# Performance work log

Measured on AMD Instinct MI355X. Metric: run time of the kernel, lower is better.

Reference implementation:

```python
import jax, jax.numpy as jnp
import numpy as np

NEG = -1e9

def gat_layer(x, edge_mask, W, al, ar, rW, b, act):
    # x: (B, N, Fin); edge_mask: (B, N, N) bool, edge u->v at [b,u,v]
    B, N, _ = x.shape
    H, D = al.shape
    f = (x @ W).reshape(B, N, H, D)                      # (B,N,H,D)
    el = jnp.einsum('bnhd,hd->bnh', f, al)               # src term
    er = jnp.einsum('bnhd,hd->bnh', f, ar)               # dst term
    # e[b,u,v,h] = LeakyReLU(el[src=u] + er[dst=v]), slope 0.2 (dgl default)
    e = jax.nn.leaky_relu(el[:, :, None, :] + er[:, None, :, :], 0.2)
    logits = jnp.where(edge_mask[..., None], e, NEG)
    # masked, empty-column-safe softmax over incoming edges (axis=1 = src u)
    m = jnp.max(logits, axis=1, keepdims=True)
    p = jnp.exp(logits - m) * edge_mask[..., None]
    alpha = p / jnp.clip(jnp.sum(p, axis=1, keepdims=True), 1e-9)
    out = jnp.einsum('buvh,buhd->bvhd', alpha, f)        # scatter-sum to dst
    res = (x @ rW).reshape(B, N, H, D)                   # residual projection
    out = out + res + b.reshape(H, D)
    return act(out) if act is not None else out


def setup_inputs() -> dict:
    key = jax.random.key(0)
    ks = jax.random.split(key, 12)
    n, c, h, w = 16, 64, 32, 32
    num_s, hid, H = 64, 64, 4
    seg = jax.random.normal(ks[0], (n, c, h, w), dtype=jnp.float32)
    adj = jax.random.normal(ks[1], (n, h * w, h * w), dtype=jnp.float32)
    s = 0.1
    return {
        'seg': seg, 'adj': adj,
        'W0': jax.random.normal(ks[2], (num_s, H * hid), dtype=jnp.float32) * s,
        'al0': jax.random.normal(ks[3], (H, hid), dtype=jnp.float32) * s,
        'ar0': jax.random.normal(ks[4], (H, hid), dtype=jnp.float32) * s,
        'rW0': jax.random.normal(ks[5], (num_s, H * hid), dtype=jnp.float32) * s,
        'b0': jnp.zeros((H * hid,), dtype=jnp.float32),
        'W1': jax.random.normal(ks[6], (H * hid, H * num_s), dtype=jnp.float32) * s,
        'al1': jax.random.normal(ks[7], (H, num_s), dtype=jnp.float32) * s,
        'ar1': jax.random.normal(ks[8], (H, num_s), dtype=jnp.float32) * s,
        'rW1': jax.random.normal(ks[9], (H * hid, H * num_s), dtype=jnp.float32) * s,
        'b1': jnp.zeros((H * num_s,), dtype=jnp.float32),
    }


def reference(seg, adj, W0, al0, ar0, rW0, b0, W1, al1, ar1, rW1, b1):
    n, c, h, w = seg.shape
    num_s = W0.shape[0]
    x = seg.reshape(n, -1, num_s)                        # (n, N, num_s)
    k = (h * w) // 6
    topv, _ = jax.lax.top_k(adj, k)
    thr = topv[..., -1]                                  # k-th largest per row
    adj_t = jnp.where(adj >= thr[..., None], adj, 0.0)
    edge_mask = adj_t > 0                                # (n, N, N)
    fea = gat_layer(x, edge_mask, W0, al0, ar0, rW0, b0, jax.nn.elu)
    fea = fea.reshape(n, fea.shape[1], -1)               # flatten heads
    fea = gat_layer(fea, edge_mask, W1, al1, ar1, rW1, b1, None)
    out = fea.mean(axis=2)                               # mean over heads -> (n, N, num_s)
    return out.reshape(n, -1, num_s)
```

## Files before the change

### kernel.cpp

```cpp
#include <hip/hip_runtime.h>
#include <hip/hip_bf16.h>
#include <stdint.h>

#define BB   16
#define NN   1024
#define KSEL 170
#define LOG2E 1.4426950408889634f

typedef __attribute__((ext_vector_type(8))) short short8;
typedef __attribute__((ext_vector_type(4))) short short4v;
typedef __attribute__((ext_vector_type(4))) float f32x4;

static __device__ __forceinline__ short f2bf(float x) {
    __hip_bfloat16 h = __float2bfloat16(x);
    return *reinterpret_cast<short*>(&h);
}
static __device__ __forceinline__ float bf2f(short x) {
    uint32_t u = ((uint32_t)(uint16_t)x) << 16;
    return __uint_as_float(u);
}
static __device__ __forceinline__ float fast_exp2(float x) {
    float r; asm("v_exp_f32 %0, %1" : "=v"(r) : "v"(x)); return r;
}

__global__ __launch_bounds__(256) void k_topk_mask(
    const float* __restrict__ adj, uint64_t* __restrict__ mask)
{
    const int wid = threadIdx.x >> 6, lane = threadIdx.x & 63;
    const int row = blockIdx.x * 4 + wid;
    const float* a = adj + (size_t)row * NN;
    __shared__ uint32_t hist[4][256];
    uint32_t* h = hist[wid];

    uint32_t key[16];
    #pragma unroll
    for (int j = 0; j < 16; ++j) {
        uint32_t u = __float_as_uint(a[lane + j * 64]);
        key[j] = u ^ ((u >> 31) ? 0xFFFFFFFFu : 0x80000000u);
    }

    uint32_t prefix = 0u, kk = KSEL;
    #pragma unroll
    for (int pass = 0; pass < 4; ++pass) {
        const int shift = 24 - 8 * pass;
        const uint32_t hi_mask = pass ? (0xFFFFFFFFu << (shift + 8)) : 0u;
        *(uint4*)&h[lane * 4] = make_uint4(0u, 0u, 0u, 0u);
        __builtin_amdgcn_wave_barrier();
        #pragma unroll
        for (int j = 0; j < 16; ++j)
            if ((key[j] & hi_mask) == prefix)
                atomicAdd(&h[(key[j] >> shift) & 255], 1u);
        __builtin_amdgcn_wave_barrier();
        const uint4 c4 = *(const uint4*)&h[lane * 4];
        const uint32_t T = c4.x + c4.y + c4.z + c4.w;
        uint32_t s = T;
        #pragma unroll
        for (int off = 1; off < 64; off <<= 1) {
            uint32_t v = __shfl_down(s, off);
            s += (lane + off < 64) ? v : 0u;
        }
        const uint32_t E = s - T;
        const uint32_t s3 = c4.w;
        const uint32_t s2 = c4.z + s3;
        const uint32_t s1 = c4.y + s2;
        const uint32_t s0 = c4.x + s1;
        const uint32_t ci[4] = {c4.x, c4.y, c4.z, c4.w};
        const uint32_t si[4] = {s0, s1, s2, s3};
        uint32_t found = 0u, nb = 0u, nk = 0u;
        #pragma unroll
        for (int i = 0; i < 4; ++i) {
            uint32_t incl = E + si[i];
            uint32_t excl = incl - ci[i];
            if (excl < kk && kk <= incl) { found = 1u; nb = (uint32_t)(lane * 4 + i); nk = kk - excl; }
        }
        uint64_t bal = __ballot(found != 0u);
        int wl = __ffsll((unsigned long long)bal) - 1;
        prefix = prefix | ((uint32_t)__shfl((int)nb, wl) << shift);
        kk = (uint32_t)__shfl((int)nk, wl);
    }

    const uint32_t thr_key = prefix;
    #pragma unroll
    for (int j = 0; j < 16; ++j) {
        bool pred = (key[j] >= thr_key) && (key[j] > 0x80000000u);
        uint64_t bal = __ballot(pred);
        if (lane == 0) mask[(size_t)row * 16 + j] = bal;
    }
}

__global__ __launch_bounds__(256) void k_maskT(
    const uint64_t* __restrict__ mask, uint64_t* __restrict__ maskT)
{
    const int tile = blockIdx.x * 4 + (threadIdx.x >> 6);
    const int lane = threadIdx.x & 63;
    const int b  = tile >> 8;
    const int uw = (tile >> 4) & 15;
    const int vw = tile & 15;
    const size_t bN = (size_t)b * NN;
    uint64_t w = mask[(bN + uw * 64 + lane) * 16 + vw];
    uint64_t r_out = 0;
    #pragma unroll
    for (int j = 0; j < 64; ++j) {
        uint64_t r = __ballot((w >> j) & 1ull);
        if (lane == j) r_out = r;
    }
    maskT[(bN + vw * 64 + lane) * 16 + uw] = r_out;
}

__global__ __launch_bounds__(256) void k_prepare(
    const float* __restrict__ W0, const float* __restrict__ rW0,
    const float* __restrict__ W1, const float* __restrict__ rW1,
    const float* __restrict__ seg,
    short* __restrict__ Wt0, short* __restrict__ rWt0,
    short* __restrict__ Wt1, short* __restrict__ rWt1,
    short* __restrict__ xb0)
{
    const int bid = blockIdx.x, t = threadIdx.x;
    if (bid < 64) {
        int idx = bid * 256 + t;
        int o = idx >> 6, k = idx & 63;
        Wt0[idx] = f2bf(W0[(size_t)k * 256 + o]);
    } else if (bid < 128) {
        int idx = (bid - 64) * 256 + t;
        int o = idx >> 6, k = idx & 63;
        rWt0[idx] = f2bf(rW0[(size_t)k * 256 + o]);
    } else if (bid < 384) {
        int idx = (bid - 128) * 256 + t;
        int o = idx >> 8, k = idx & 255;
        Wt1[idx] = f2bf(W1[(size_t)k * 256 + o]);
    } else if (bid < 640) {
        int idx = (bid - 384) * 256 + t;
        int o = idx >> 8, k = idx & 255;
        rWt1[idx] = f2bf(rW1[(size_t)k * 256 + o]);
    } else {
        int i = ((bid - 640) * 256 + t) * 4;
        float4 v = *(const float4*)(seg + i);
        short4v o4;
        o4[0] = f2bf(v.x); o4[1] = f2bf(v.y); o4[2] = f2bf(v.z); o4[3] = f2bf(v.w);
        *(short4v*)(xb0 + i) = o4;
    }
}

template<int K>
__global__ __launch_bounds__(256, 2) void k_features_mfma(
    const short* __restrict__ xb,
    const short* __restrict__ Wt,
    const short* __restrict__ rWt,
    const float* __restrict__ al,
    const float* __restrict__ ar,
    short* __restrict__ ft,
    short* __restrict__ fea,
    float* __restrict__ el_t,
    float* __restrict__ er_t)
{
    const int tid = threadIdx.x, lane = tid & 63, hh = tid >> 6;
    const int l15 = lane & 15, l4 = lane >> 4;
    const int n0 = blockIdx.x * 32;
    const int b_idx = n0 >> 10;
    const int nloc = n0 & (NN - 1);
    const int bh = b_idx * 4 + hh;
    const int XP = K + 8;

    __shared__ short x_lds[32 * (K + 8)];

    const int CH = K / 8;
    #pragma unroll
    for (int c = tid; c < 32 * CH; c += 256) {
        const int row = c / CH, col = c - row * CH;
        *(short8*)&x_lds[row * XP + col * 8] =
            *(const short8*)(xb + ((size_t)n0 + row) * K + col * 8);
    }
    __syncthreads();

    const short* wbase = Wt  + (size_t)(hh * 64 + l15) * K + l4 * 8;
    const short* rbase = rWt + (size_t)(hh * 64 + l15) * K + l4 * 8;
    const size_t qs = (size_t)16 * K;

    f32x4 accf[2][4], accr[2][4];
    #pragma unroll
    for (int s = 0; s < 2; ++s)
        #pragma unroll
        for (int q = 0; q < 4; ++q) {
            accf[s][q] = (f32x4){0.f, 0.f, 0.f, 0.f};
            accr[s][q] = (f32x4){0.f, 0.f, 0.f, 0.f};
        }

    short8 bufW[2][4], bufR[2][4];
    #pragma unroll
    for (int q = 0; q < 4; ++q) {
        bufW[0][q] = *(const short8*)(wbase + q * qs);
        bufR[0][q] = *(const short8*)(rbase + q * qs);
    }

    #pragma unroll
    for (int ks = 0; ks < K / 32; ++ks) {
        const int cur = ks & 1, nxt = cur ^ 1;
        if (ks + 1 < K / 32) {
            #pragma unroll
            for (int q = 0; q < 4; ++q) {
                bufW[nxt][q] = *(const short8*)(wbase + q * qs + (ks + 1) * 32);
                bufR[nxt][q] = *(const short8*)(rbase + q * qs + (ks + 1) * 32);
            }
            __builtin_amdgcn_sched_barrier(0);
        }
        short8 x0 = *(const short8*)&x_lds[l15 * XP + ks * 32 + l4 * 8];
        short8 x1 = *(const short8*)&x_lds[(16 + l15) * XP + ks * 32 + l4 * 8];
        #pragma unroll
        for (int q = 0; q < 4; ++q) {
            accf[0][q] = __builtin_amdgcn_mfma_f32_16x16x32_bf16(x0, bufW[cur][q], accf[0][q], 0, 0, 0);
            accf[1][q] = __builtin_amdgcn_mfma_f32_16x16x32_bf16(x1, bufW[cur][q], accf[1][q], 0, 0, 0);
            accr[0][q] = __builtin_amdgcn_mfma_f32_16x16x32_bf16(bufR[cur][q], x0, accr[0][q], 0, 0, 0);
            accr[1][q] = __builtin_amdgcn_mfma_f32_16x16x32_bf16(bufR[cur][q], x1, accr[1][q], 0, 0, 0);
        }
    }

    #pragma unroll
    for (int s = 0; s < 2; ++s) {
        const int nl = nloc + s * 16;
        #pragma unroll
        for (int q = 0; q < 4; ++q) {
            short4v pk;
            #pragma unroll
            for (int r = 0; r < 4; ++r) pk[r] = f2bf(accf[s][q][r]);
            const int dl = q * 16 + l15;
            const size_t idx = ((size_t)bh << 16)
                             + (size_t)(nl >> 6) * 4096
                             + (size_t)(((nl & 63) >> 3) + (l4 >> 1)) * 512
                             + (size_t)dl * 8 + (l4 & 1) * 4;
            *(short4v*)(ft + idx) = pk;
        }
        float elv[4] = {0.f, 0.f, 0.f, 0.f}, erv[4] = {0.f, 0.f, 0.f, 0.f};
        #pragma unroll
        for (int q = 0; q < 4; ++q) {
            const float alv = al[hh * 64 + q * 16 + l15];
            const float arv = ar[hh * 64 + q * 16 + l15];
            #pragma unroll
            for (int r = 0; r < 4; ++r) {
                elv[r] = fmaf(accf[s][q][r], alv, elv[r]);
                erv[r] = fmaf(accf[s][q][r], arv, erv[r]);
            }
        }
        #pragma unroll
        for (int r = 0; r < 4; ++r) {
            #pragma unroll
            for (int off = 1; off < 16; off <<= 1) {
                elv[r] += __shfl_xor(elv[r], off);
                erv[r] += __shfl_xor(erv[r], off);
            }
        }
        if (l15 == 0) {
            float4 e4, r4;
            e4.x = elv[0] * LOG2E; e4.y = elv[1] * LOG2E;
            e4.z = elv[2] * LOG2E; e4.w = elv[3] * LOG2E;
            r4.x = erv[0] * LOG2E; r4.y = erv[1] * LOG2E;
            r4.z = erv[2] * LOG2E; r4.w = erv[3] * LOG2E;
            *(float4*)(el_t + (size_t)bh * NN + nl + l4 * 4) = e4;
            *(float4*)(er_t + (size_t)bh * NN + nl + l4 * 4) = r4;
        }
        #pragma unroll
        for (int q = 0; q < 4; ++q) {
            short4v pk;
            #pragma unroll
            for (int r = 0; r < 4; ++r) pk[r] = f2bf(accr[s][q][r]);
            *(short4v*)(fea + ((size_t)n0 + s * 16 + l15) * 256 + hh * 64 + q * 16 + l4 * 4) = pk;
        }
    }
}

template<int ELU_ON>
__global__ __launch_bounds__(256, 4) void k_attn(
    const short* __restrict__ ft,
    const float* __restrict__ el_t,
    const float* __restrict__ er_t,
    const uint64_t* __restrict__ maskT,
    const float* __restrict__ bias,
    short* fea)
{
    const int id = blockIdx.x;
    const int swz = (id & 7) * 64 + (id >> 3);
    const int b  = swz >> 5;
    const int h  = (swz >> 3) & 3;
    const int vt = swz & 7;
    const int tid = threadIdx.x;
    const int lane = tid & 63, wid = tid >> 6;
    const int l15 = lane & 15, l4 = lane >> 4;
    const int bh = b * 4 + h;
    const size_t bN = (size_t)b * NN;
    const int v0 = vt * 128;

    __shared__ __align__(16) short f_lds[2][4096];
    __shared__ __align__(16) float el_lds[NN];
    __shared__ __align__(16) uint64_t m_lds[128 * 17];
    __shared__ float smax[4];

    const short* gsrc = ft + ((size_t)bh << 16);

    {
        short8 sa = *(const short8*)(gsrc + tid * 8);
        short8 sb = *(const short8*)(gsrc + 2048 + tid * 8);
        float4 ev4 = ((const float4*)(el_t + (size_t)bh * NN))[tid];
        ((float4*)el_lds)[tid] = ev4;
        float m = fmaxf(fmaxf(ev4.x, ev4.y), fmaxf(ev4.z, ev4.w));
        #pragma unroll
        for (int off = 32; off; off >>= 1) m = fmaxf(m, __shfl_xor(m, off));
        if (lane == 0) smax[wid] = m;
        #pragma unroll
        for (int i = 0; i < 8; ++i) {
            int idx = tid + i * 256;
            m_lds[(idx >> 4) * 17 + (idx & 15)] =
                maskT[(bN + v0 + (idx >> 4)) * 16 + (idx & 15)];
        }
        *(short8*)&f_lds[0][tid * 8] = sa;
        *(short8*)&f_lds[0][2048 + tid * 8] = sb;
    }

    const int vlo = wid * 32 + l15, vhi = vlo + 16;
    const float er_lo = er_t[(size_t)bh * NN + v0 + vlo];
    const float er_hi = er_t[(size_t)bh * NN + v0 + vhi];

    __syncthreads();

    const float emx = fmaxf(fmaxf(smax[0], smax[1]), fmaxf(smax[2], smax[3]));
    const float e0 = emx + er_lo;
    const float cv_lo = fmaxf(e0, 0.2f * e0);
    const float e1 = emx + er_hi;
    const float cv_hi = fmaxf(e1, 0.2f * e1);
    const float c1_lo = er_lo - cv_lo, c2_lo = 0.2f * er_lo - cv_lo;
    const float c1_hi = er_hi - cv_hi, c2_hi = 0.2f * er_hi - cv_hi;

    const uint8_t* mbytes = (const uint8_t*)m_lds;
    const int moff_lo = vlo * 136, moff_hi = vhi * 136;

    short8 ones8;
    #pragma unroll
    for (int i = 0; i < 8; ++i) ones8[i] = (short)0x3F80;

    f32x4 accLo[4], accHi[4];
    #pragma unroll
    for (int i = 0; i < 4; ++i) {
        accLo[i] = (f32x4){0.f, 0.f, 0.f, 0.f};
        accHi[i] = (f32x4){0.f, 0.f, 0.f, 0.f};
    }
    f32x4 dLo = (f32x4){0.f, 0.f, 0.f, 0.f};
    f32x4 dHi = (f32x4){0.f, 0.f, 0.f, 0.f};

    short8 Ra, Rb;
    #pragma unroll 1
    for (int tt = 0; tt < 16; ++tt) {
        if (tt < 15) {
            Ra = *(const short8*)(gsrc + (tt + 1) * 4096 + tid * 8);
            Rb = *(const short8*)(gsrc + (tt + 1) * 4096 + 2048 + tid * 8);
            __builtin_amdgcn_sched_barrier(0);
        }
        const short* fb = f_lds[tt & 1];
        #pragma unroll
        for (int kc = 0; kc < 2; ++kc) {
            const float* ep = &el_lds[tt * 64 + kc * 32 + l4 * 8];
            float4 ev0 = *(const float4*)ep;
            float4 ev1 = *(const float4*)(ep + 4);
            const float ev[8] = {ev0.x, ev0.y, ev0.z, ev0.w, ev1.x, ev1.y, ev1.z, ev1.w};
            uint32_t mLo = mbytes[moff_lo + tt * 8 + kc * 4 + l4];
            uint32_t mHi = mbytes[moff_hi + tt * 8 + kc * 4 + l4];
            short8 aLo, aHi;
            #pragma unroll
            for (int j = 0; j < 8; ++j) {
                float e = ev[j];
                float argL = fmaxf(e + c1_lo, fmaf(0.2f, e, c2_lo));
                float argH = fmaxf(e + c1_hi, fmaf(0.2f, e, c2_hi));
                float pL = ((mLo >> j) & 1u) ? fast_exp2(argL) : 0.f;
                float pH = ((mHi >> j) & 1u) ? fast_exp2(argH) : 0.f;
                aLo[j] = f2bf(pL);
                aHi[j] = f2bf(pH);
            }
            const int fo = (kc * 4 + l4) * 512 + l15 * 8;
            short8 bw0 = *(const short8*)(fb + fo);
            short8 bw1 = *(const short8*)(fb + fo + 128);
            short8 bw2 = *(const short8*)(fb + fo + 256);
            short8 bw3 = *(const short8*)(fb + fo + 384);
            __builtin_amdgcn_s_setprio(1);
            accLo[0] = __builtin_amdgcn_mfma_f32_16x16x32_bf16(aLo, bw0, accLo[0], 0, 0, 0);
            accLo[1] = __builtin_amdgcn_mfma_f32_16x16x32_bf16(aLo, bw1, accLo[1], 0, 0, 0);
            accLo[2] = __builtin_amdgcn_mfma_f32_16x16x32_bf16(aLo, bw2, accLo[2], 0, 0, 0);
            accLo[3] = __builtin_amdgcn_mfma_f32_16x16x32_bf16(aLo, bw3, accLo[3], 0, 0, 0);
            dLo      = __builtin_amdgcn_mfma_f32_16x16x32_bf16(aLo, ones8, dLo, 0, 0, 0);
            accHi[0] = __builtin_amdgcn_mfma_f32_16x16x32_bf16(aHi, bw0, accHi[0], 0, 0, 0);
            accHi[1] = __builtin_amdgcn_mfma_f32_16x16x32_bf16(aHi, bw1, accHi[1], 0, 0, 0);
            accHi[2] = __builtin_amdgcn_mfma_f32_16x16x32_bf16(aHi, bw2, accHi[2], 0, 0, 0);
            accHi[3] = __builtin_amdgcn_mfma_f32_16x16x32_bf16(aHi, bw3, accHi[3], 0, 0, 0);
            dHi      = __builtin_amdgcn_mfma_f32_16x16x32_bf16(aHi, ones8, dHi, 0, 0, 0);
            __builtin_amdgcn_s_setprio(0);
        }
        if (tt < 15) {
            *(short8*)&f_lds[(tt + 1) & 1][tid * 8] = Ra;
            *(short8*)&f_lds[(tt + 1) & 1][2048 + tid * 8] = Rb;
        }
        __syncthreads();
    }

    float rcpLo[4], rcpHi[4];
    #pragma unroll
    for (int r = 0; r < 4; ++r) {
        rcpLo[r] = 1.f / fmaxf(dLo[r], 1e-9f);
        rcpHi[r] = 1.f / fmaxf(dHi[r], 1e-9f);
    }
    #pragma unroll
    for (int dt = 0; dt < 4; ++dt) {
        const int d = dt * 16 + l15;
        const float bv = bias[h * 64 + d];
        #pragma unroll
        for (int r = 0; r < 4; ++r) {
            const int vl = v0 + wid * 32 + l4 * 4 + r;
            const size_t rowL = (bN + vl) * 256 + h * 64 + d;
            float ov = accLo[dt][r] * rcpLo[r] + bf2f(fea[rowL]) + bv;
            if (ELU_ON) ov = ov > 0.f ? ov : __expf(ov) - 1.f;
            fea[rowL] = f2bf(ov);
            const size_t rowH = (bN + vl + 16) * 256 + h * 64 + d;
            float ov2 = accHi[dt][r] * rcpHi[r] + bf2f(fea[rowH]) + bv;
            if (ELU_ON) ov2 = ov2 > 0.f ? ov2 : __expf(ov2) - 1.f;
            fea[rowH] = f2bf(ov2);
        }
    }
}

__global__ __launch_bounds__(256) void k_headmean(
    const short* __restrict__ fea, float* __restrict__ outp)
{
    int i = blockIdx.x * 256 + threadIdx.x;
    int d = i & 63;
    size_t node = (size_t)(i >> 6);
    const short* p = fea + node * 256;
    outp[i] = 0.25f * (bf2f(p[d]) + bf2f(p[64 + d]) + bf2f(p[128 + d]) + bf2f(p[192 + d]));
}

extern "C" void kernel_launch(void* const* d_in, const int* in_sizes, int n_in,
                              void* d_out, int out_size, void* d_ws, size_t ws_size,
                              hipStream_t stream) {
    const float* seg = (const float*)d_in[0];
    const float* adj = (const float*)d_in[1];
    const float* W0  = (const float*)d_in[2];
    const float* al0 = (const float*)d_in[3];
    const float* ar0 = (const float*)d_in[4];
    const float* rW0 = (const float*)d_in[5];
    const float* b0  = (const float*)d_in[6];
    const float* W1  = (const float*)d_in[7];
    const float* al1 = (const float*)d_in[8];
    const float* ar1 = (const float*)d_in[9];
    const float* rW1 = (const float*)d_in[10];
    const float* b1  = (const float*)d_in[11];
    float* out = (float*)d_out;

    char* ws = (char*)d_ws;
    size_t off = 0;
    uint64_t* mask  = (uint64_t*)ws;
    off += (size_t)BB * NN * 16 * 8;
    uint64_t* maskT = (uint64_t*)(ws + off); off += (size_t)BB * NN * 16 * 8;
    short* ftb = (short*)(ws + off); off += (size_t)BB * 256 * NN * 2;
    short* fea = (short*)(ws + off); off += (size_t)BB * NN * 256 * 2;
    short* xb0 = (short*)(ws + off); off += (size_t)BB * NN * 64 * 2;
    char* r0 = (char*)mask;
    short* Wt0  = (short*)r0;                 r0 += 256 * 64 * 2;
    short* rWt0 = (short*)r0;                 r0 += 256 * 64 * 2;
    short* Wt1  = (short*)r0;                 r0 += 256 * 256 * 2;
    short* rWt1 = (short*)r0;                 r0 += 256 * 256 * 2;
    float* el   = (float*)r0;                 r0 += (size_t)BB * 4 * NN * 4;
    float* er   = (float*)r0;                 r0 += (size_t)BB * 4 * NN * 4;

    k_topk_mask<<<BB * NN / 4, 256, 0, stream>>>(adj, mask);
    k_maskT<<<BB * 256 / 4, 256, 0, stream>>>(mask, maskT);
    k_prepare<<<640 + BB * NN * 64 / 1024, 256, 0, stream>>>(
        W0, rW0, W1, rW1, seg, Wt0, rWt0, Wt1, rWt1, xb0);

    k_features_mfma<64><<<BB * NN / 32, 256, 0, stream>>>(xb0, Wt0, rWt0, al0, ar0,
                                                          ftb, fea, el, er);
    k_attn<1><<<512, 256, 0, stream>>>(ftb, el, er, maskT, b0, fea);
    k_features_mfma<256><<<BB * NN / 32, 256, 0, stream>>>(fea, Wt1, rWt1, al1, ar1,
                                                           ftb, fea, el, er);
    k_attn<0><<<512, 256, 0, stream>>>(ftb, el, er, maskT, b1, fea);

    k_headmean<<<BB * NN * 64 / 256, 256, 0, stream>>>(fea, out);
}
```

Before: 159.4 us.

## Shorten topk radix select and halve attention tile per block

The top-k threshold search now runs only two 8-bit radix histogram passes. It then resolves the remaining low 16 bits by repeated wave-wide max-and-count over the candidates that share the prefix, which avoids two histogram passes. The attention kernel now processes 64 destination nodes per block instead of 128 and launches 1024 blocks, giving more parallelism and fewer registers per thread. In exchange, each feature tile is streamed from global memory twice as often. The iterative max loop could also run many times if many keys share the 16-bit prefix.

```diff
diff --git a/kernel.cpp b/kernel.cpp
--- a/kernel.cpp
+++ b/kernel.cpp
@@ -41,9 +41,9 @@
 
     uint32_t prefix = 0u, kk = KSEL;
     #pragma unroll
-    for (int pass = 0; pass < 4; ++pass) {
+    for (int pass = 0; pass < 2; ++pass) {
         const int shift = 24 - 8 * pass;
-        const uint32_t hi_mask = pass ? (0xFFFFFFFFu << (shift + 8)) : 0u;
+        const uint32_t hi_mask = pass ? 0xFF000000u : 0u;
         *(uint4*)&h[lane * 4] = make_uint4(0u, 0u, 0u, 0u);
         __builtin_amdgcn_wave_barrier();
         #pragma unroll
@@ -79,7 +79,34 @@
         kk = (uint32_t)__shfl((int)nk, wl);
     }
 
-    const uint32_t thr_key = prefix;
+    uint32_t sv[16];
+    #pragma unroll
+    for (int j = 0; j < 16; ++j)
+        sv[j] = ((key[j] ^ prefix) >> 16) == 0u ? key[j] : 0u;
+
+    uint32_t thr_key;
+    for (;;) {
+        uint32_t m = 0u;
+        #pragma unroll
+        for (int j = 0; j < 16; ++j) m = m > sv[j] ? m : sv[j];
+        #pragma unroll
+        for (int off = 1; off < 64; off <<= 1) {
+            uint32_t v = __shfl_xor(m, off);
+            m = m > v ? m : v;
+        }
+        if (m == 0u) { thr_key = 0u; break; }
+        uint32_t c = 0u;
+        #pragma unroll
+        for (int j = 0; j < 16; ++j) c += (sv[j] == m) ? 1u : 0u;
+        #pragma unroll
+        for (int off = 1; off < 64; off <<= 1)
+            c += __shfl_xor(c, off);
+        if (kk <= c) { thr_key = m; break; }
+        kk -= c;
+        #pragma unroll
+        for (int j = 0; j < 16; ++j) if (sv[j] == m) sv[j] = 0u;
+    }
+
     #pragma unroll
     for (int j = 0; j < 16; ++j) {
         bool pred = (key[j] >= thr_key) && (key[j] > 0x80000000u);
@@ -277,20 +304,20 @@
     short* fea)
 {
     const int id = blockIdx.x;
-    const int swz = (id & 7) * 64 + (id >> 3);
-    const int b  = swz >> 5;
-    const int h  = (swz >> 3) & 3;
-    const int vt = swz & 7;
+    const int swz = (id & 7) * 128 + (id >> 3);
+    const int b  = swz >> 6;
+    const int h  = (swz >> 4) & 3;
+    const int vt = swz & 15;
     const int tid = threadIdx.x;
     const int lane = tid & 63, wid = tid >> 6;
     const int l15 = lane & 15, l4 = lane >> 4;
     const int bh = b * 4 + h;
     const size_t bN = (size_t)b * NN;
-    const int v0 = vt * 128;
+    const int v0 = vt * 64;
 
     __shared__ __align__(16) short f_lds[2][4096];
     __shared__ __align__(16) float el_lds[NN];
-    __shared__ __align__(16) uint64_t m_lds[128 * 17];
+    __shared__ __align__(16) uint64_t m_lds[64 * 17];
     __shared__ float smax[4];
 
     const short* gsrc = ft + ((size_t)bh << 16);
@@ -305,7 +332,7 @@
         for (int off = 32; off; off >>= 1) m = fmaxf(m, __shfl_xor(m, off));
         if (lane == 0) smax[wid] = m;
         #pragma unroll
-        for (int i = 0; i < 8; ++i) {
+        for (int i = 0; i < 4; ++i) {
             int idx = tid + i * 256;
             m_lds[(idx >> 4) * 17 + (idx & 15)] =
                 maskT[(bN + v0 + (idx >> 4)) * 16 + (idx & 15)];
@@ -314,35 +341,27 @@
         *(short8*)&f_lds[0][2048 + tid * 8] = sb;
     }
 
-    const int vlo = wid * 32 + l15, vhi = vlo + 16;
+    const int vlo = wid * 16 + l15;
     const float er_lo = er_t[(size_t)bh * NN + v0 + vlo];
-    const float er_hi = er_t[(size_t)bh * NN + v0 + vhi];
 
     __syncthreads();
 
     const float emx = fmaxf(fmaxf(smax[0], smax[1]), fmaxf(smax[2], smax[3]));
     const float e0 = emx + er_lo;
     const float cv_lo = fmaxf(e0, 0.2f * e0);
-    const float e1 = emx + er_hi;
-    const float cv_hi = fmaxf(e1, 0.2f * e1);
     const float c1_lo = er_lo - cv_lo, c2_lo = 0.2f * er_lo - cv_lo;
-    const float c1_hi = er_hi - cv_hi, c2_hi = 0.2f * er_hi - cv_hi;
 
     const uint8_t* mbytes = (const uint8_t*)m_lds;
-    const int moff_lo = vlo * 136, moff_hi = vhi * 136;
+    const int moff_lo = vlo * 136;
 
     short8 ones8;
     #pragma unroll
     for (int i = 0; i < 8; ++i) ones8[i] = (short)0x3F80;
 
-    f32x4 accLo[4], accHi[4];
-    #pragma unroll
-    for (int i = 0; i < 4; ++i) {
-        accLo[i] = (f32x4){0.f, 0.f, 0.f, 0.f};
-        accHi[i] = (f32x4){0.f, 0.f, 0.f, 0.f};
-    }
+    f32x4 accLo[4];
+    #pragma unroll
+    for (int i = 0; i < 4; ++i) accLo[i] = (f32x4){0.f, 0.f, 0.f, 0.f};
     f32x4 dLo = (f32x4){0.f, 0.f, 0.f, 0.f};
-    f32x4 dHi = (f32x4){0.f, 0.f, 0.f, 0.f};
 
     short8 Ra, Rb;
     #pragma unroll 1
@@ -360,17 +379,13 @@
             float4 ev1 = *(const float4*)(ep + 4);
             const float ev[8] = {ev0.x, ev0.y, ev0.z, ev0.w, ev1.x, ev1.y, ev1.z, ev1.w};
             uint32_t mLo = mbytes[moff_lo + tt * 8 + kc * 4 + l4];
-            uint32_t mHi = mbytes[moff_hi + tt * 8 + kc * 4 + l4];
-            short8 aLo, aHi;
+            short8 aLo;
             #pragma unroll
             for (int j = 0; j < 8; ++j) {
                 float e = ev[j];
                 float argL = fmaxf(e + c1_lo, fmaf(0.2f, e, c2_lo));
-                float argH = fmaxf(e + c1_hi, fmaf(0.2f, e, c2_hi));
                 float pL = ((mLo >> j) & 1u) ? fast_exp2(argL) : 0.f;
-                float pH = ((mHi >> j) & 1u) ? fast_exp2(argH) : 0.f;
                 aLo[j] = f2bf(pL);
-                aHi[j] = f2bf(pH);
             }
             const int fo = (kc * 4 + l4) * 512 + l15 * 8;
             short8 bw0 = *(const short8*)(fb + fo);
@@ -383,11 +398,6 @@
             accLo[2] = __builtin_amdgcn_mfma_f32_16x16x32_bf16(aLo, bw2, accLo[2], 0, 0, 0);
             accLo[3] = __builtin_amdgcn_mfma_f32_16x16x32_bf16(aLo, bw3, accLo[3], 0, 0, 0);
             dLo      = __builtin_amdgcn_mfma_f32_16x16x32_bf16(aLo, ones8, dLo, 0, 0, 0);
-            accHi[0] = __builtin_amdgcn_mfma_f32_16x16x32_bf16(aHi, bw0, accHi[0], 0, 0, 0);
-            accHi[1] = __builtin_amdgcn_mfma_f32_16x16x32_bf16(aHi, bw1, accHi[1], 0, 0, 0);
-            accHi[2] = __builtin_amdgcn_mfma_f32_16x16x32_bf16(aHi, bw2, accHi[2], 0, 0, 0);
-            accHi[3] = __builtin_amdgcn_mfma_f32_16x16x32_bf16(aHi, bw3, accHi[3], 0, 0, 0);
-            dHi      = __builtin_amdgcn_mfma_f32_16x16x32_bf16(aHi, ones8, dHi, 0, 0, 0);
             __builtin_amdgcn_s_setprio(0);
         }
         if (tt < 15) {
@@ -397,27 +407,21 @@
         __syncthreads();
     }
 
-    float rcpLo[4], rcpHi[4];
-    #pragma unroll
-    for (int r = 0; r < 4; ++r) {
+    float rcpLo[4];
+    #pragma unroll
+    for (int r = 0; r < 4; ++r)
         rcpLo[r] = 1.f / fmaxf(dLo[r], 1e-9f);
-        rcpHi[r] = 1.f / fmaxf(dHi[r], 1e-9f);
-    }
     #pragma unroll
     for (int dt = 0; dt < 4; ++dt) {
         const int d = dt * 16 + l15;
         const float bv = bias[h * 64 + d];
         #pragma unroll
         for (int r = 0; r < 4; ++r) {
-            const int vl = v0 + wid * 32 + l4 * 4 + r;
+            const int vl = v0 + wid * 16 + l4 * 4 + r;
             const size_t rowL = (bN + vl) * 256 + h * 64 + d;
             float ov = accLo[dt][r] * rcpLo[r] + bf2f(fea[rowL]) + bv;
             if (ELU_ON) ov = ov > 0.f ? ov : __expf(ov) - 1.f;
             fea[rowL] = f2bf(ov);
-            const size_t rowH = (bN + vl + 16) * 256 + h * 64 + d;
-            float ov2 = accHi[dt][r] * rcpHi[r] + bf2f(fea[rowH]) + bv;
-            if (ELU_ON) ov2 = ov2 > 0.f ? ov2 : __expf(ov2) - 1.f;
-            fea[rowH] = f2bf(ov2);
         }
     }
 }
@@ -472,10 +476,10 @@
 
     k_features_mfma<64><<<BB * NN / 32, 256, 0, stream>>>(xb0, Wt0, rWt0, al0, ar0,
                                                           ftb, fea, el, er);
-    k_attn<1><<<512, 256, 0, stream>>>(ftb, el, er, maskT, b0, fea);
+    k_attn<1><<<1024, 256, 0, stream>>>(ftb, el, er, maskT, b0, fea);
     k_features_mfma<256><<<BB * NN / 32, 256, 0, stream>>>(fea, Wt1, rWt1, al1, ar1,
                                                            ftb, fea, el, er);
-    k_attn<0><<<512, 256, 0, stream>>>(ftb, el, er, maskT, b1, fea);
+    k_attn<0><<<1024, 256, 0, stream>>>(ftb, el, er, maskT, b1, fea);
 
     k_headmean<<<BB * NN * 64 / 256, 256, 0, stream>>>(fea, out);
 }
```

Result: faster. 153.4 us (-3.8%).
